# Optimization experiments

Measured on AMD Instinct MI355X. Metric: run time of the kernel, lower is better.

The kernel has to match this reference:

```python
import jax, jax.numpy as jnp
import numpy as np

EMBED_DIM = 1024
NUM_HEADS = 16
PROJ_DIM = EMBED_DIM // NUM_HEADS


def setup_inputs() -> dict:
    key = jax.random.key(0)
    ks = jax.random.split(key, 9)
    s = 1.0 / np.sqrt(EMBED_DIM)
    inp = {
        "inputs": jax.random.normal(ks[0], (4, 2048, EMBED_DIM), dtype=jnp.float32),
        "Wq": jax.random.normal(ks[1], (EMBED_DIM, EMBED_DIM), dtype=jnp.float32) * s,
        "bq": jnp.zeros((EMBED_DIM,), jnp.float32),
        "Wk": jax.random.normal(ks[2], (EMBED_DIM, EMBED_DIM), dtype=jnp.float32) * s,
        "bk": jnp.zeros((EMBED_DIM,), jnp.float32),
        "Wv": jax.random.normal(ks[3], (EMBED_DIM, EMBED_DIM), dtype=jnp.float32) * s,
        "bv": jnp.zeros((EMBED_DIM,), jnp.float32),
        "Wo": jax.random.normal(ks[4], (EMBED_DIM, EMBED_DIM), dtype=jnp.float32) * s,
        "bo": jnp.zeros((EMBED_DIM,), jnp.float32),
    }
    return inp


def _split_heads(x):
    # [B, S, E] -> [B, H, S, D]
    b, s, _ = x.shape
    return x.reshape(b, s, NUM_HEADS, PROJ_DIM).transpose(0, 2, 1, 3)


def reference(inputs, Wq, bq, Wk, bk, Wv, bv, Wo, bo):
    q = _split_heads(inputs @ Wq + bq)
    k = _split_heads(inputs @ Wk + bk)
    v = _split_heads(inputs @ Wv + bv)
    scale = 1.0 / jnp.sqrt(jnp.asarray(PROJ_DIM, inputs.dtype))
    scores = jnp.einsum("bhqd,bhkd->bhqk", q, k) * scale  # [B,H,S,S]
    weights = jax.nn.softmax(scores, axis=-1)
    attn = jnp.einsum("bhqk,bhkd->bhqd", weights, v)
    b, h, s, d = attn.shape
    concat = attn.transpose(0, 2, 1, 3).reshape(b, s, h * d)
    return concat @ Wo + bo
```

## Files before the change

kernel.cpp:

```cpp
#include <hip/hip_runtime.h>
#include <math.h>

#define EMB 1024
#define SEQ 2048
#define BATCH 4
#define NH 16
#define HD 64
#define MTOT (BATCH * SEQ)

typedef _Float16 half_t;
typedef _Float16 half8 __attribute__((ext_vector_type(8)));
typedef __fp16 fp16x2 __attribute__((ext_vector_type(2)));
typedef float floatx4 __attribute__((ext_vector_type(4)));
typedef float floatx16 __attribute__((ext_vector_type(16)));

#if __has_builtin(__builtin_amdgcn_exp2f)
#define EXP2(x) __builtin_amdgcn_exp2f(x)
#else
#define EXP2(x) exp2f(x)
#endif

#define QSCALE 0.18033688f

#define GLOAD16(gsrc, ldst)                                                   \
  __builtin_amdgcn_global_load_lds(                                           \
      (__attribute__((address_space(1))) void*)(gsrc),                        \
      (__attribute__((address_space(3))) void*)(ldst), 16, 0, 0)

__device__ __forceinline__ unsigned pkh(float a, float b) {
  union { fp16x2 h; unsigned u; } c;
  c.h = __builtin_amdgcn_cvt_pkrtz(a, b);
  return c.u;
}

__global__ __launch_bounds__(256) void conv_all(const float* __restrict__ x,
                                                half_t* __restrict__ xh,
                                                const float* __restrict__ W0,
                                                const float* __restrict__ W1,
                                                const float* __restrict__ W2,
                                                const float* __restrict__ W3,
                                                half_t* __restrict__ wt) {
  __shared__ float T[64][68];
  const int bid = blockIdx.x;
  const int t = threadIdx.x;
  if (bid < 4096) {
    int i = bid * 256 + t;
    float4 a = ((const float4*)x)[i * 2];
    float4 b = ((const float4*)x)[i * 2 + 1];
    float v[8] = {a.x, a.y, a.z, a.w, b.x, b.y, b.z, b.w};
    half8 o;
#pragma unroll
    for (int j = 0; j < 8; ++j) o[j] = (half_t)v[j];
    *(half8*)(xh + (size_t)i * 8) = o;
    return;
  }
  const int b2 = bid - 4096;
  const int z = b2 >> 8, rem = b2 & 255;
  const int k0 = (rem >> 4) * 64, n0 = (rem & 15) * 64;
  const float* W = (z == 0) ? W0 : (z == 1) ? W1 : (z == 2) ? W2 : W3;
  half_t* wto = wt + (size_t)z * 1048576;
#pragma unroll
  for (int i = 0; i < 4; ++i) {
    int idx = t + i * 256;
    int row = idx >> 4, c4 = (idx & 15) << 2;
    *(float4*)(&T[row][c4]) = *(const float4*)(W + (size_t)(k0 + row) * EMB + n0 + c4);
  }
  __syncthreads();
#pragma unroll
  for (int cc = 0; cc < 2; ++cc) {
    int c = t + cc * 256;
    int n = c >> 3, g = c & 7;
    half8 hh;
#pragma unroll
    for (int j = 0; j < 8; ++j) hh[j] = (half_t)T[g * 8 + j][n];
    *(half8*)(wto + (size_t)(n0 + n) * EMB + k0 + g * 8) = hh;
  }
}

__global__ __launch_bounds__(256) void gemm_qkv(const half_t* __restrict__ A,
                                                const half_t* __restrict__ WT,
                                                const float* __restrict__ bq,
                                                const float* __restrict__ bk,
                                                const float* __restrict__ bvv,
                                                half_t* __restrict__ Qh,
                                                half_t* __restrict__ Kh,
                                                half_t* __restrict__ Vt) {
  __shared__ half_t lds[17536];
  half_t* As = lds;
  half_t* Bs = lds + 4096;

  const int mat = blockIdx.x;
  const half_t* B = WT + (size_t)mat * 1048576;
  const float* bias = (mat == 0) ? bq : (mat == 1) ? bk : bvv;
  const float scale = (mat == 0) ? QSCALE : 1.0f;
  half_t* outh = (mat == 0) ? Qh : (mat == 1) ? Kh : Vt;

  const int t = threadIdx.x;
  const int l = t & 63, w = t >> 6;
  const int wm = w >> 1, wn = w & 1;
  const int lr = l & 15, lg = l >> 4;
  const int row0 = blockIdx.y * 128, col0 = blockIdx.z * 128;

  const int sr2 = (w << 4) + (l >> 2);
  const int swz = (l & 3) ^ (sr2 & 3);
  const int rdsw = (lg ^ (lr & 3)) << 3;

  floatx4 acc[4][4];
#pragma unroll
  for (int i = 0; i < 4; ++i)
#pragma unroll
    for (int j = 0; j < 4; ++j) acc[i][j] = (floatx4){0.f, 0.f, 0.f, 0.f};

  for (int kb = 0; kb < EMB; kb += 32) {
    __syncthreads();
    GLOAD16(A + (size_t)(row0 + sr2) * EMB + kb + swz * 8, As + ((w << 4) << 5));
    GLOAD16(A + (size_t)(row0 + 64 + sr2) * EMB + kb + swz * 8,
            As + ((64 + (w << 4)) << 5));
    GLOAD16(B + (size_t)(col0 + sr2) * EMB + kb + swz * 8, Bs + ((w << 4) << 5));
    GLOAD16(B + (size_t)(col0 + 64 + sr2) * EMB + kb + swz * 8,
            Bs + ((64 + (w << 4)) << 5));
    __syncthreads();

    half8 fa[4];
#pragma unroll
    for (int mf = 0; mf < 4; ++mf)
      fa[mf] = *(const half8*)(As + ((wm * 64 + mf * 16 + lr) << 5) + rdsw);
#pragma unroll
    for (int nf = 0; nf < 4; ++nf) {
      half8 fb = *(const half8*)(Bs + ((wn * 64 + nf * 16 + lr) << 5) + rdsw);
#pragma unroll
      for (int mf = 0; mf < 4; ++mf)
        acc[mf][nf] = __builtin_amdgcn_mfma_f32_16x16x32_f16(fa[mf], fb, acc[mf][nf], 0, 0, 0);
    }
  }

  float bv[4];
#pragma unroll
  for (int nf = 0; nf < 4; ++nf) bv[nf] = bias[col0 + wn * 64 + nf * 16 + lr];

  if (mat < 2) {
#pragma unroll
    for (int mf = 0; mf < 4; ++mf)
#pragma unroll
      for (int nf = 0; nf < 4; ++nf)
#pragma unroll
        for (int r = 0; r < 4; ++r) {
          int row = row0 + wm * 64 + mf * 16 + lg * 4 + r;
          int col = col0 + wn * 64 + nf * 16 + lr;
          int bb = row >> 11, ss = row & (SEQ - 1);
          int hh = col >> 6, dd = col & (HD - 1);
          float f = (acc[mf][nf][r] + bv[nf]) * scale;
          outh[((size_t)(bb * NH + hh) * SEQ + ss) * HD + dd] = (half_t)f;
        }
  } else {
    half_t* T = lds;
    const int bb = row0 >> 11, s0 = row0 & (SEQ - 1);
    __syncthreads();
#pragma unroll
    for (int mf = 0; mf < 4; ++mf)
#pragma unroll
      for (int nf = 0; nf < 4; ++nf)
#pragma unroll
        for (int r = 0; r < 4; ++r) {
          float f = acc[mf][nf][r] + bv[nf];
          T[(wm * 64 + mf * 16 + lg * 4 + r) * 137 + wn * 64 + nf * 16 + lr] = (half_t)f;
        }
    __syncthreads();
#pragma unroll
    for (int i = 0; i < 8; ++i) {
      int idx = t + i * 256;
      int n = idx >> 4, mg = idx & 15;
      int col = col0 + n;
      int hh = col >> 6, dd = col & (HD - 1);
      half8 pk;
#pragma unroll
      for (int j = 0; j < 8; ++j) pk[j] = T[(mg * 8 + j) * 137 + n];
      *(half8*)(outh + ((size_t)(bb * NH + hh) * HD + dd) * SEQ + s0 + mg * 8) = pk;
    }
  }
}

__global__ __launch_bounds__(256) void gemmo(const half_t* __restrict__ A,
                                             const half_t* __restrict__ B,
                                             const float* __restrict__ bias,
                                             float* __restrict__ outf) {
  __shared__ half_t lds[8192];
  half_t* As = lds;
  half_t* Bs = lds + 4096;

  const int t = threadIdx.x;
  const int l = t & 63, w = t >> 6;
  const int wm = w >> 1, wn = w & 1;
  const int lr = l & 15, lg = l >> 4;
  const int row0 = blockIdx.x * 128, col0 = blockIdx.y * 128;
  const int sr2 = (w << 4) + (l >> 2);
  const int swz = (l & 3) ^ (sr2 & 3);
  const int rdsw = (lg ^ (lr & 3)) << 3;

  floatx4 acc[4][4];
#pragma unroll
  for (int i = 0; i < 4; ++i)
#pragma unroll
    for (int j = 0; j < 4; ++j) acc[i][j] = (floatx4){0.f, 0.f, 0.f, 0.f};

  for (int kb = 0; kb < EMB; kb += 32) {
    __syncthreads();
    GLOAD16(A + (size_t)(row0 + sr2) * EMB + kb + swz * 8, As + ((w << 4) << 5));
    GLOAD16(A + (size_t)(row0 + 64 + sr2) * EMB + kb + swz * 8,
            As + ((64 + (w << 4)) << 5));
    GLOAD16(B + (size_t)(col0 + sr2) * EMB + kb + swz * 8, Bs + ((w << 4) << 5));
    GLOAD16(B + (size_t)(col0 + 64 + sr2) * EMB + kb + swz * 8,
            Bs + ((64 + (w << 4)) << 5));
    __syncthreads();

    half8 fa[4];
#pragma unroll
    for (int mf = 0; mf < 4; ++mf)
      fa[mf] = *(const half8*)(As + ((wm * 64 + mf * 16 + lr) << 5) + rdsw);
#pragma unroll
    for (int nf = 0; nf < 4; ++nf) {
      half8 fb = *(const half8*)(Bs + ((wn * 64 + nf * 16 + lr) << 5) + rdsw);
#pragma unroll
      for (int mf = 0; mf < 4; ++mf)
        acc[mf][nf] = __builtin_amdgcn_mfma_f32_16x16x32_f16(fa[mf], fb, acc[mf][nf], 0, 0, 0);
    }
  }

  float bv[4];
#pragma unroll
  for (int nf = 0; nf < 4; ++nf) bv[nf] = bias[col0 + wn * 64 + nf * 16 + lr];
#pragma unroll
  for (int mf = 0; mf < 4; ++mf)
#pragma unroll
    for (int nf = 0; nf < 4; ++nf)
#pragma unroll
      for (int r = 0; r < 4; ++r) {
        int row = row0 + wm * 64 + mf * 16 + lg * 4 + r;
        int col = col0 + wn * 64 + nf * 16 + lr;
        outf[(size_t)row * EMB + col] = acc[mf][nf][r] + bv[nf];
      }
}

__global__ __launch_bounds__(512) void attnh(const half_t* __restrict__ Q,
                                             const half_t* __restrict__ K,
                                             const half_t* __restrict__ Vt,
                                             half_t* __restrict__ att) {
  __shared__ half_t lds[4 * 4608];

  const int t = threadIdx.x, l = t & 63, wq = t >> 6;
  const int lq = l & 31, hi = l >> 5;
  const int hi8 = hi * 8, hi4 = hi * 4;
  const int bh = blockIdx.x;
  const int q0 = blockIdx.y * 256;
  const size_t kbase = (size_t)bh * SEQ * HD;
  const size_t vbase = (size_t)bh * HD * SEQ;
  const int srow = t >> 3, sg = t & 7;
  const int soff = srow * 72 + sg * 8;

  half8 qf[4];
  const int qrow = q0 + wq * 32 + lq;
#pragma unroll
  for (int s = 0; s < 4; ++s)
    qf[s] = *(const half8*)(Q + kbase + (size_t)qrow * HD + s * 16 + hi8);

  floatx16 o0, o1;
#pragma unroll
  for (int r = 0; r < 16; ++r) { o0[r] = 0.f; o1[r] = 0.f; }
  float l_s = 0.f;

  half8 kh_r = *(const half8*)(K + kbase + (size_t)srow * HD + sg * 8);
  half8 vh_r = *(const half8*)(Vt + vbase + (size_t)srow * SEQ + sg * 8);
  *(half8*)(lds + soff) = kh_r;
  *(half8*)(lds + 4608 + soff) = vh_r;
  kh_r = *(const half8*)(K + kbase + (size_t)(64 + srow) * HD + sg * 8);
  vh_r = *(const half8*)(Vt + vbase + (size_t)srow * SEQ + 64 + sg * 8);
  __syncthreads();

  for (int it = 0; it < SEQ / 64; ++it) {
    const int cur = it & 1;
    half_t* Kb = lds + (cur ? 9216 : 0);
    half_t* Vb = Kb + 4608;
    half_t* Kw = lds + (cur ? 0 : 9216);
    half_t* Vw = Kw + 4608;

    *(half8*)(Kw + soff) = kh_r;
    *(half8*)(Vw + soff) = vh_r;

    {
      int nk = ((it + 2) * 64) & (SEQ - 1);
      kh_r = *(const half8*)(K + kbase + (size_t)(nk + srow) * HD + sg * 8);
      vh_r = *(const half8*)(Vt + vbase + (size_t)srow * SEQ + nk + sg * 8);
    }

    floatx16 s0v, s1v;
#pragma unroll
    for (int r = 0; r < 16; ++r) { s0v[r] = 0.f; s1v[r] = 0.f; }
    __builtin_amdgcn_s_setprio(1);
#pragma unroll
    for (int s = 0; s < 4; ++s) {
      const int off = s * 16 + hi8;
      half8 kf0 = *(const half8*)(Kb + lq * 72 + off);
      half8 kf1 = *(const half8*)(Kb + (32 + lq) * 72 + off);
      s0v = __builtin_amdgcn_mfma_f32_32x32x16_f16(kf0, qf[s], s0v, 0, 0, 0);
      s1v = __builtin_amdgcn_mfma_f32_32x32x16_f16(kf1, qf[s], s1v, 0, 0, 0);
    }
    __builtin_amdgcn_s_setprio(0);

    float rsum = 0.f;
#pragma unroll
    for (int r = 0; r < 16; ++r) { s0v[r] = EXP2(s0v[r]); rsum += s0v[r]; }
#pragma unroll
    for (int r = 0; r < 16; ++r) { s1v[r] = EXP2(s1v[r]); rsum += s1v[r]; }
    rsum += __shfl_xor(rsum, 32);
    l_s += rsum;

#define PV_STEP(SC, RH, S)                                                    \
  {                                                                           \
    unsigned u0 = pkh(SC[(RH) * 8 + 0], SC[(RH) * 8 + 1]);                    \
    unsigned u1 = pkh(SC[(RH) * 8 + 2], SC[(RH) * 8 + 3]);                    \
    unsigned u2 = pkh(SC[(RH) * 8 + 4], SC[(RH) * 8 + 5]);                    \
    unsigned u3 = pkh(SC[(RH) * 8 + 6], SC[(RH) * 8 + 7]);                    \
    asm volatile("v_permlane32_swap_b32 %0, %1" : "+v"(u0), "+v"(u2));        \
    asm volatile("v_permlane32_swap_b32 %0, %1" : "+v"(u1), "+v"(u3));        \
    int4 pi = make_int4((int)u0, (int)u1, (int)u2, (int)u3);                  \
    half8 pa = *(half8*)&pi;                                                  \
    half8 vb0 = *(const half8*)(Vb + lq * 72 + (S) * 16 + hi8);               \
    half8 vb1 = *(const half8*)(Vb + (32 + lq) * 72 + (S) * 16 + hi8);        \
    __builtin_amdgcn_s_setprio(1);                                            \
    o0 = __builtin_amdgcn_mfma_f32_32x32x16_f16(pa, vb0, o0, 0, 0, 0);        \
    o1 = __builtin_amdgcn_mfma_f32_32x32x16_f16(pa, vb1, o1, 0, 0, 0);        \
    __builtin_amdgcn_s_setprio(0);                                            \
  }
    PV_STEP(s0v, 0, 0)
    PV_STEP(s0v, 1, 1)
    PV_STEP(s1v, 0, 2)
    PV_STEP(s1v, 1, 3)
#undef PV_STEP

    __syncthreads();
  }

  float inv = 1.f / l_s;
  float il[16];
#pragma unroll
  for (int r = 0; r < 16; ++r)
    il[r] = __shfl(inv, ((r & 3) + 8 * (r >> 2)) + hi4);
  const int bb2 = bh >> 4, hh2 = bh & 15;
#pragma unroll
  for (int r = 0; r < 16; ++r) {
    int qg = q0 + wq * 32 + ((r & 3) + 8 * (r >> 2)) + hi4;
    size_t off = ((size_t)bb2 * SEQ + qg) * EMB + hh2 * HD + lq;
    att[off] = (half_t)(o0[r] * il[r]);
    att[off + 32] = (half_t)(o1[r] * il[r]);
  }
}

extern "C" void kernel_launch(void* const* d_in, const int* in_sizes, int n_in,
                              void* d_out, int out_size, void* d_ws, size_t ws_size,
                              hipStream_t stream) {
  const float* X  = (const float*)d_in[0];
  const float* Wq = (const float*)d_in[1];
  const float* bq = (const float*)d_in[2];
  const float* Wk = (const float*)d_in[3];
  const float* bk = (const float*)d_in[4];
  const float* Wv = (const float*)d_in[5];
  const float* bv = (const float*)d_in[6];
  const float* Wo = (const float*)d_in[7];
  const float* bo = (const float*)d_in[8];
  float* out = (float*)d_out;

  char* wsb = (char*)d_ws;
  const size_t MB = 1024 * 1024;
  half_t* Xh = (half_t*)(wsb);
  half_t* WT = (half_t*)(wsb + 17 * MB);
  half_t* Qh = (half_t*)(wsb + 26 * MB);
  half_t* Kh = (half_t*)(wsb + 43 * MB);
  half_t* Vt = (half_t*)d_out;
  half_t* att = Xh;

  half_t* WTq = WT;
  half_t* WTo = WT + 3145728;

  conv_all<<<dim3(5120), 256, 0, stream>>>(X, Xh, Wq, Wk, Wv, Wo, WT);

  gemm_qkv<<<dim3(3, MTOT / 128, EMB / 128), 256, 0, stream>>>(
      Xh, WTq, bq, bk, bv, Qh, Kh, Vt);

  attnh<<<dim3(BATCH * NH, SEQ / 256), 512, 0, stream>>>(Qh, Kh, Vt, att);

  gemmo<<<dim3(MTOT / 128, EMB / 128), 256, 0, stream>>>(att, WTo, bo, out);
}
```

Measured before the change: 195.6 us.

## Halve attention block size and accumulate softmax row sums in packed fp16

The attention kernel now runs 256-thread blocks covering 128 queries instead of 512 threads covering 256, which doubles the grid. Each thread loads two K/V rows per tile so the 64-key staging into LDS stays complete. The per-iteration softmax denominator is now summed with packed fp16 adds on the already-converted probabilities instead of 32 scalar fp32 adds. This cuts VALU work, but fp16 accumulation over 32 values per tile loses some precision in the normaliser. Smaller blocks also mean each K/V tile is reloaded by twice as many blocks.

```diff
diff --git a/kernel.cpp b/kernel.cpp
--- a/kernel.cpp
+++ b/kernel.cpp
@@ -241,7 +241,7 @@
       }
 }
 
-__global__ __launch_bounds__(512) void attnh(const half_t* __restrict__ Q,
+__global__ __launch_bounds__(256) void attnh(const half_t* __restrict__ Q,
                                              const half_t* __restrict__ K,
                                              const half_t* __restrict__ Vt,
                                              half_t* __restrict__ att) {
@@ -251,11 +251,12 @@
   const int lq = l & 31, hi = l >> 5;
   const int hi8 = hi * 8, hi4 = hi * 4;
   const int bh = blockIdx.x;
-  const int q0 = blockIdx.y * 256;
+  const int q0 = blockIdx.y * 128;
   const size_t kbase = (size_t)bh * SEQ * HD;
   const size_t vbase = (size_t)bh * HD * SEQ;
   const int srow = t >> 3, sg = t & 7;
-  const int soff = srow * 72 + sg * 8;
+  const int soff0 = srow * 72 + sg * 8;
+  const int soff1 = (srow + 32) * 72 + sg * 8;
 
   half8 qf[4];
   const int qrow = q0 + wq * 32 + lq;
@@ -268,12 +269,18 @@
   for (int r = 0; r < 16; ++r) { o0[r] = 0.f; o1[r] = 0.f; }
   float l_s = 0.f;
 
-  half8 kh_r = *(const half8*)(K + kbase + (size_t)srow * HD + sg * 8);
-  half8 vh_r = *(const half8*)(Vt + vbase + (size_t)srow * SEQ + sg * 8);
-  *(half8*)(lds + soff) = kh_r;
-  *(half8*)(lds + 4608 + soff) = vh_r;
-  kh_r = *(const half8*)(K + kbase + (size_t)(64 + srow) * HD + sg * 8);
-  vh_r = *(const half8*)(Vt + vbase + (size_t)srow * SEQ + 64 + sg * 8);
+  half8 kh_a = *(const half8*)(K + kbase + (size_t)srow * HD + sg * 8);
+  half8 kh_b = *(const half8*)(K + kbase + (size_t)(srow + 32) * HD + sg * 8);
+  half8 vh_a = *(const half8*)(Vt + vbase + (size_t)srow * SEQ + sg * 8);
+  half8 vh_b = *(const half8*)(Vt + vbase + (size_t)(srow + 32) * SEQ + sg * 8);
+  *(half8*)(lds + soff0) = kh_a;
+  *(half8*)(lds + soff1) = kh_b;
+  *(half8*)(lds + 4608 + soff0) = vh_a;
+  *(half8*)(lds + 4608 + soff1) = vh_b;
+  kh_a = *(const half8*)(K + kbase + (size_t)(64 + srow) * HD + sg * 8);
+  kh_b = *(const half8*)(K + kbase + (size_t)(96 + srow) * HD + sg * 8);
+  vh_a = *(const half8*)(Vt + vbase + (size_t)srow * SEQ + 64 + sg * 8);
+  vh_b = *(const half8*)(Vt + vbase + (size_t)(srow + 32) * SEQ + 64 + sg * 8);
   __syncthreads();
 
   for (int it = 0; it < SEQ / 64; ++it) {
@@ -283,13 +290,17 @@
     half_t* Kw = lds + (cur ? 0 : 9216);
     half_t* Vw = Kw + 4608;
 
-    *(half8*)(Kw + soff) = kh_r;
-    *(half8*)(Vw + soff) = vh_r;
+    *(half8*)(Kw + soff0) = kh_a;
+    *(half8*)(Kw + soff1) = kh_b;
+    *(half8*)(Vw + soff0) = vh_a;
+    *(half8*)(Vw + soff1) = vh_b;
 
     {
       int nk = ((it + 2) * 64) & (SEQ - 1);
-      kh_r = *(const half8*)(K + kbase + (size_t)(nk + srow) * HD + sg * 8);
-      vh_r = *(const half8*)(Vt + vbase + (size_t)srow * SEQ + nk + sg * 8);
+      kh_a = *(const half8*)(K + kbase + (size_t)(nk + srow) * HD + sg * 8);
+      kh_b = *(const half8*)(K + kbase + (size_t)(nk + srow + 32) * HD + sg * 8);
+      vh_a = *(const half8*)(Vt + vbase + (size_t)srow * SEQ + nk + sg * 8);
+      vh_b = *(const half8*)(Vt + vbase + (size_t)(srow + 32) * SEQ + nk + sg * 8);
     }
 
     floatx16 s0v, s1v;
@@ -306,13 +317,12 @@
     }
     __builtin_amdgcn_s_setprio(0);
 
-    float rsum = 0.f;
-#pragma unroll
-    for (int r = 0; r < 16; ++r) { s0v[r] = EXP2(s0v[r]); rsum += s0v[r]; }
-#pragma unroll
-    for (int r = 0; r < 16; ++r) { s1v[r] = EXP2(s1v[r]); rsum += s1v[r]; }
-    rsum += __shfl_xor(rsum, 32);
-    l_s += rsum;
+#pragma unroll
+    for (int r = 0; r < 16; ++r) s0v[r] = EXP2(s0v[r]);
+#pragma unroll
+    for (int r = 0; r < 16; ++r) s1v[r] = EXP2(s1v[r]);
+
+    fp16x2 psum = {(__fp16)0.f, (__fp16)0.f};
 
 #define PV_STEP(SC, RH, S)                                                    \
   {                                                                           \
@@ -320,6 +330,8 @@
     unsigned u1 = pkh(SC[(RH) * 8 + 2], SC[(RH) * 8 + 3]);                    \
     unsigned u2 = pkh(SC[(RH) * 8 + 4], SC[(RH) * 8 + 5]);                    \
     unsigned u3 = pkh(SC[(RH) * 8 + 6], SC[(RH) * 8 + 7]);                    \
+    union { unsigned u; fp16x2 h; } a0{u0}, a1{u1}, a2{u2}, a3{u3};           \
+    psum += (a0.h + a1.h) + (a2.h + a3.h);                                    \
     asm volatile("v_permlane32_swap_b32 %0, %1" : "+v"(u0), "+v"(u2));        \
     asm volatile("v_permlane32_swap_b32 %0, %1" : "+v"(u1), "+v"(u3));        \
     int4 pi = make_int4((int)u0, (int)u1, (int)u2, (int)u3);                  \
@@ -336,6 +348,10 @@
     PV_STEP(s1v, 0, 2)
     PV_STEP(s1v, 1, 3)
 #undef PV_STEP
+
+    float ts = (float)psum[0] + (float)psum[1];
+    ts += __shfl_xor(ts, 32);
+    l_s += ts;
 
     __syncthreads();
   }
@@ -386,7 +402,7 @@
   gemm_qkv<<<dim3(3, MTOT / 128, EMB / 128), 256, 0, stream>>>(
       Xh, WTq, bq, bk, bv, Qh, Kh, Vt);
 
-  attnh<<<dim3(BATCH * NH, SEQ / 256), 512, 0, stream>>>(Qh, Kh, Vt, att);
+  attnh<<<dim3(BATCH * NH, SEQ / 128), 256, 0, stream>>>(Qh, Kh, Vt, att);
 
   gemmo<<<dim3(MTOT / 128, EMB / 128), 256, 0, stream>>>(att, WTo, bo, out);
 }
```

Result: slower. 214.0 us (+9.4%).
